# Optimization experiments

Hardware: AMD Instinct MI355X
Metric: run time of the kernel (lower is better)

The kernel has to match this reference:

```python
import jax, jax.numpy as jnp
import numpy as np

D_MODEL, N_LAYER, VOCAB = 1024, 4, 50280
D_INNER, D_STATE, D_CONV, DT_RANK = 2048, 16, 4, 64
B, L = 1, 1024
EPS = 1e-5


def _rmsnorm(x, w):
    var = jnp.mean(jnp.square(x), axis=-1, keepdims=True)
    return x * jax.lax.rsqrt(var + EPS) * w


def _selective_scan(u, dt, A, Bm, Cm, Dv):
    # u, dt: [b,l,d]; A: [d,n]; Bm, Cm: [b,l,n]; Dv: [d]
    dA = jnp.exp(dt[..., None] * A)                      # [b,l,d,n]
    dBu = dt[..., None] * Bm[:, :, None, :] * u[..., None]  # [b,l,d,n]

    def step(s, x):
        dA_t, dBu_t, C_t = x
        s = s * dA_t + dBu_t                             # [b,d,n]
        y = jnp.einsum('bdn,bn->bd', s, C_t)
        return s, y

    s0 = jnp.zeros((u.shape[0], u.shape[2], A.shape[1]), u.dtype)
    xs = (dA.transpose(1, 0, 2, 3), dBu.transpose(1, 0, 2, 3), Cm.transpose(1, 0, 2))
    _, ys = jax.lax.scan(step, s0, xs)                   # ys: [l,b,d]
    return ys.transpose(1, 0, 2) + u * Dv


def _mixer(x, in_w, cw, cb, xp_w, dt_w, dt_b, A_log, Dv, out_w):
    Lx = x.shape[1]
    xz = jnp.einsum('bld,ed->ble', x, in_w)              # [b,l,2*d_inner]
    xp, z = jnp.split(xz, 2, axis=-1)
    # causal depthwise conv1d, kernel size D_CONV
    xpad = jnp.pad(xp, ((0, 0), (D_CONV - 1, 0), (0, 0)))
    conv = cb + sum(xpad[:, k:k + Lx, :] * cw[:, k] for k in range(D_CONV))
    u = jax.nn.silu(conv)
    xdbl = jnp.einsum('bld,ed->ble', u, xp_w)            # [b,l,dt_rank+2n]
    dt_r = xdbl[..., :DT_RANK]
    Bm = xdbl[..., DT_RANK:DT_RANK + D_STATE]
    Cm = xdbl[..., DT_RANK + D_STATE:]
    dt = jax.nn.softplus(jnp.einsum('blr,dr->bld', dt_r, dt_w) + dt_b)
    A = -jnp.exp(A_log)
    y = _selective_scan(u, dt, A, Bm, Cm, Dv)
    y = y * jax.nn.silu(z)
    return jnp.einsum('bld,ed->ble', y, out_w)


def _forward(input_ids, embedding, norm_w, in_proj_w, conv_w, conv_b, x_proj_w,
             dt_proj_w, dt_proj_b, A_log, D, out_proj_w, norm_f_w):
    hidden = embedding[input_ids]                        # [b,l,d_model]
    residual = None
    for i in range(N_LAYER):
        residual = hidden if residual is None else hidden + residual
        x = _rmsnorm(residual, norm_w[i])
        hidden = _mixer(x, in_proj_w[i], conv_w[i], conv_b[i], x_proj_w[i],
                        dt_proj_w[i], dt_proj_b[i], A_log[i], D[i], out_proj_w[i])
    residual = hidden + residual
    hf = _rmsnorm(residual, norm_f_w)
    # lm_head weight is tied to embedding
    return jnp.einsum('bld,vd->blv', hf, embedding)


def setup_inputs() -> dict:
    key = jax.random.key(0)
    ks = jax.random.split(key, 8)
    s = 0.02
    return {
        'input_ids': jax.random.randint(ks[0], (B, L), 0, VOCAB),
        'embedding': jax.random.normal(ks[1], (VOCAB, D_MODEL), jnp.float32) * s,
        'norm_w': jnp.ones((N_LAYER, D_MODEL), jnp.float32),
        'in_proj_w': jax.random.normal(ks[2], (N_LAYER, 2 * D_INNER, D_MODEL), jnp.float32) * s,
        'conv_w': jax.random.normal(ks[3], (N_LAYER, D_INNER, D_CONV), jnp.float32) * s,
        'conv_b': jnp.zeros((N_LAYER, D_INNER), jnp.float32),
        'x_proj_w': jax.random.normal(ks[4], (N_LAYER, DT_RANK + 2 * D_STATE, D_INNER), jnp.float32) * s,
        'dt_proj_w': jax.random.normal(ks[5], (N_LAYER, D_INNER, DT_RANK), jnp.float32) * s,
        'dt_proj_b': jnp.full((N_LAYER, D_INNER), -4.6, jnp.float32),  # softplus ~= 0.01
        'A_log': jnp.tile(jnp.log(jnp.arange(1.0, D_STATE + 1.0, dtype=jnp.float32))[None, None, :],
                          (N_LAYER, D_INNER, 1)),
        'D': jnp.ones((N_LAYER, D_INNER), jnp.float32),
        'out_proj_w': jax.random.normal(ks[6], (N_LAYER, D_MODEL, D_INNER), jnp.float32) * s,
        'norm_f_w': jnp.ones((D_MODEL,), jnp.float32),
    }


def reference(input_ids, embedding, norm_w, in_proj_w, conv_w, conv_b, x_proj_w,
              dt_proj_w, dt_proj_b, A_log, D, out_proj_w, norm_f_w):
    return _forward(input_ids, embedding, norm_w, in_proj_w, conv_w, conv_b,
                    x_proj_w, dt_proj_w, dt_proj_b, A_log, D, out_proj_w, norm_f_w)
```

## Files before the change

### kernel.cpp

```cpp
#include <hip/hip_runtime.h>
#include <hip/hip_bf16.h>

#define D_MODEL 1024
#define N_LAYER 4
#define D_INNER 2048
#define D_STATE 16
#define D_CONV  4
#define DT_RANK 64
#define SEQ_L   1024
#define VOCAB   50280
#define VOCAB_PAD 50304
#define NCHUNK  32
#define CLEN    32

typedef __attribute__((ext_vector_type(8))) short short8;
typedef __attribute__((ext_vector_type(4))) float f32x4;

typedef __attribute__((address_space(1))) const unsigned GUint;
typedef __attribute__((address_space(3))) unsigned LUint;

__device__ __forceinline__ float silu_f(float x) {
    return x / (1.0f + __expf(-x));
}
__device__ __forceinline__ float softplus_f(float x) {
    return fmaxf(x, 0.0f) + log1pf(__expf(-fabsf(x)));
}
__device__ __forceinline__ ushort f2bf(float f) {
    union { float f; unsigned u; } uf; uf.f = f;
    unsigned r = uf.u + 0x7FFF + ((uf.u >> 16) & 1);
    return (ushort)(r >> 16);
}

__global__ void f32_to_bf16_kernel(const float* __restrict__ in,
                                   ushort* __restrict__ out, int n4) {
    int i = blockIdx.x * 256 + threadIdx.x;
    if (i >= n4) return;
    float4 v = *(const float4*)(in + (size_t)i * 4);
    ushort4 o;
    o.x = f2bf(v.x); o.y = f2bf(v.y); o.z = f2bf(v.z); o.w = f2bf(v.w);
    *(ushort4*)(out + (size_t)i * 4) = o;
}

__global__ void xpw_convert_kernel(const float* __restrict__ src,
                                   ushort* __restrict__ dst) {
    int q = blockIdx.x * 256 + threadIdx.x;
    int layer = q / (128 * 512);
    int rq    = q % (128 * 512);
    int row   = rq / 512;
    int cq    = rq % 512;
    ushort4 o;
    if (row < 96) {
        float4 v = *(const float4*)(src + ((size_t)layer * 96 + row) * 2048 + cq * 4);
        o.x = f2bf(v.x); o.y = f2bf(v.y); o.z = f2bf(v.z); o.w = f2bf(v.w);
    } else {
        o.x = o.y = o.z = o.w = 0;
    }
    *(ushort4*)(dst + (size_t)q * 4) = o;
}

__global__ void embed_kernel(const int* __restrict__ ids,
                             const float* __restrict__ emb,
                             float* __restrict__ hidden) {
    int l = blockIdx.x;
    int t = threadIdx.x;
    int id = ids[l];
    float4 v = *(const float4*)(emb + (size_t)id * D_MODEL + t * 4);
    *(float4*)(hidden + (size_t)l * D_MODEL + t * 4) = v;
}

__global__ void add_rmsnorm_kernel(float* __restrict__ res,
                                   const float* __restrict__ part,
                                   const float* __restrict__ w,
                                   ushort* __restrict__ xout,
                                   int add, int nparts) {
    int l = blockIdx.x;
    int t = threadIdx.x;
    size_t base = (size_t)l * D_MODEL + t * 4;
    float4 r;
    if (add) r = *(const float4*)(res + base);
    else     r = make_float4(0.f, 0.f, 0.f, 0.f);
    for (int s = 0; s < nparts; ++s) {
        float4 hv = *(const float4*)(part + (size_t)s * SEQ_L * D_MODEL + base);
        r.x += hv.x; r.y += hv.y; r.z += hv.z; r.w += hv.w;
    }
    *(float4*)(res + base) = r;
    float ss = r.x * r.x + r.y * r.y + r.z * r.z + r.w * r.w;
    #pragma unroll
    for (int off = 32; off > 0; off >>= 1) ss += __shfl_down(ss, off, 64);
    __shared__ float sred[4];
    if ((t & 63) == 0) sred[t >> 6] = ss;
    __syncthreads();
    float tot = sred[0] + sred[1] + sred[2] + sred[3];
    float scale = rsqrtf(tot * (1.0f / (float)D_MODEL) + 1e-5f);
    float4 wv = *(const float4*)(w + t * 4);
    ushort4 o;
    o.x = f2bf(r.x * scale * wv.x);
    o.y = f2bf(r.y * scale * wv.y);
    o.z = f2bf(r.z * scale * wv.z);
    o.w = f2bf(r.w * scale * wv.w);
    *(ushort4*)(xout + base) = o;
}

template<int SPLIT>
__global__ void gemm_bf16_gld_kernel(const ushort* __restrict__ A,
                                     const ushort* __restrict__ W,
                                     float* __restrict__ C,
                                     int N, int K, int lda, int ldc,
                                     int MB, int KS, int pstride) {
    __shared__ ushort As[2][128][32];
    __shared__ ushort Ws[2][128][32];
    const int t  = threadIdx.x;
    const int T  = gridDim.x >> 3;
    const int id = blockIdx.x;
    const int j  = (id & 7) * T + (id >> 3);
    const int ks  = j % KS;
    const int rem = j / KS;
    const int m0 = (rem % MB) * 128;
    const int n0 = (rem / MB) * 128;
    const int kchunk = K / KS;
    const int kbeg = ks * kchunk;
    const int kend = kbeg + kchunk;

    const int lane = t & 63;
    const int w    = t >> 6;
    const int srow = w * 16 + (lane >> 2);
    const int scol = (((lane & 3) ^ ((lane >> 3) & 3)) * 8);
    const ushort* Ag0 = A + (size_t)(m0 + srow) * lda + scol;
    const ushort* Ag1 = A + (size_t)(m0 + srow + 64) * lda + scol;
    const ushort* Wg0 = W + (size_t)(n0 + srow) * K + scol;
    const ushort* Wg1 = W + (size_t)(n0 + srow + 64) * K + scol;

    const int wm = (t >> 7) & 1;
    const int wn = (t >> 6) & 1;
    const int lr = lane & 15;
    const int lk = lane >> 4;
    const int swz = (lr >> 1) & 3;

    f32x4 acc[4][4] = {};

#define STAGE_GLD(buf, kk)                                                        \
    do {                                                                          \
        __builtin_amdgcn_global_load_lds((GUint*)(Ag0 + (kk)),                    \
            (LUint*)&As[buf][w * 16][0], 16, 0, 0);                               \
        __builtin_amdgcn_global_load_lds((GUint*)(Ag1 + (kk)),                    \
            (LUint*)&As[buf][64 + w * 16][0], 16, 0, 0);                          \
        __builtin_amdgcn_global_load_lds((GUint*)(Wg0 + (kk)),                    \
            (LUint*)&Ws[buf][w * 16][0], 16, 0, 0);                               \
        __builtin_amdgcn_global_load_lds((GUint*)(Wg1 + (kk)),                    \
            (LUint*)&Ws[buf][64 + w * 16][0], 16, 0, 0);                          \
    } while (0)

    STAGE_GLD(0, kbeg);
    int buf = 0;
    for (int k0 = kbeg;;) {
        __syncthreads();
        const bool more = (k0 + 32) < kend;
        if (more) STAGE_GLD(buf ^ 1, k0 + 32);

        short8 af[4], bfr[4];
        #pragma unroll
        for (int m = 0; m < 4; ++m)
            af[m] = *(const short8*)&As[buf][wm * 64 + m * 16 + lr][(lk ^ swz) * 8];
        #pragma unroll
        for (int n = 0; n < 4; ++n)
            bfr[n] = *(const short8*)&Ws[buf][wn * 64 + n * 16 + lr][(lk ^ swz) * 8];
        #pragma unroll
        for (int m = 0; m < 4; ++m)
            #pragma unroll
            for (int n = 0; n < 4; ++n)
                acc[m][n] = __builtin_amdgcn_mfma_f32_16x16x32_bf16(
                    af[m], bfr[n], acc[m][n], 0, 0, 0);

        if (!more) break;
        buf ^= 1;
        k0 += 32;
    }
#undef STAGE_GLD

    float* Cp = SPLIT ? (C + (size_t)ks * pstride) : C;
    #pragma unroll
    for (int m = 0; m < 4; ++m) {
        const int row = m0 + wm * 64 + m * 16 + lk * 4;
        #pragma unroll
        for (int n = 0; n < 4; ++n) {
            const int col = n0 + wn * 64 + n * 16 + lr;
            if (col < N) {
                #pragma unroll
                for (int r = 0; r < 4; ++r)
                    Cp[(size_t)(row + r) * ldc + col] = acc[m][n][r];
            }
        }
    }
}

__global__ void xdbl_reduce_kernel(const float* __restrict__ part,
                                   float* __restrict__ out,
                                   ushort* __restrict__ dtr_b) {
    int i = blockIdx.x * 256 + threadIdx.x;
    float4 acc = make_float4(0.f, 0.f, 0.f, 0.f);
    #pragma unroll
    for (int s = 0; s < 32; ++s) {
        float4 v = *(const float4*)(part + (size_t)s * SEQ_L * 96 + (size_t)i * 4);
        acc.x += v.x; acc.y += v.y; acc.z += v.z; acc.w += v.w;
    }
    *(float4*)(out + (size_t)i * 4) = acc;
    int c = (i * 4) % 96;
    if (c < 64) {
        int r = (i * 4) / 96;
        ushort4 o;
        o.x = f2bf(acc.x); o.y = f2bf(acc.y); o.z = f2bf(acc.z); o.w = f2bf(acc.w);
        *(ushort4*)(dtr_b + (size_t)r * 64 + c) = o;
    }
}

__global__ void conv_silu_kernel(const float* __restrict__ xz,
                                 const float* __restrict__ cw,
                                 const float* __restrict__ cb,
                                 float* __restrict__ u,
                                 ushort* __restrict__ u_b) {
    int idx = blockIdx.x * 256 + threadIdx.x;
    int l = idx >> 11;
    int c = idx & 2047;
    float acc = cb[c];
    float w0 = cw[c * 4 + 0], w1 = cw[c * 4 + 1], w2 = cw[c * 4 + 2], w3 = cw[c * 4 + 3];
#define XP(ll) (xz[(size_t)(ll) * 4096 + c] + xz[(size_t)SEQ_L * 4096 + (size_t)(ll) * 4096 + c])
    if (l >= 3) acc = fmaf(XP(l - 3), w0, acc);
    if (l >= 2) acc = fmaf(XP(l - 2), w1, acc);
    if (l >= 1) acc = fmaf(XP(l - 1), w2, acc);
    acc = fmaf(XP(l), w3, acc);
#undef XP
    float s = silu_f(acc);
    u[idx] = s;
    u_b[idx] = f2bf(s);
}

__global__ void scan_a_kernel(const float* __restrict__ u,
                              const float* __restrict__ dtp,
                              const float* __restrict__ dt_bias,
                              const float* __restrict__ xdbl,
                              const float* __restrict__ A_log,
                              float* __restrict__ yloc,
                              float* __restrict__ cumdt,
                              float* __restrict__ s_end) {
    const int idx = blockIdx.x * 256 + threadIdx.x;
    const int d = idx & 2047;
    const int c = idx >> 11;

    float Aa[16];
    #pragma unroll
    for (int q = 0; q < 4; ++q) {
        float4 al = *(const float4*)(A_log + (size_t)d * 16 + q * 4);
        Aa[q * 4 + 0] = -__expf(al.x);
        Aa[q * 4 + 1] = -__expf(al.y);
        Aa[q * 4 + 2] = -__expf(al.z);
        Aa[q * 4 + 3] = -__expf(al.w);
    }
    const float dbias = dt_bias[d];

    float s[16];
    #pragma unroll
    for (int n = 0; n < 16; ++n) s[n] = 0.0f;
    float cd = 0.0f;

    const int l0 = c * CLEN;
    for (int i = 0; i < CLEN; ++i) {
        const int l = l0 + i;
        const float dtl = softplus_f(dtp[(size_t)l * 2048 + d]
                                   + dtp[(size_t)SEQ_L * 2048 + (size_t)l * 2048 + d]
                                   + dbias);
        const float ul  = u[(size_t)l * 2048 + d];
        float Bn[16], Cn[16];
        const float* xbp = xdbl + (size_t)l * 96;
        *(float4*)&Bn[0]  = *(const float4*)(xbp + 64);
        *(float4*)&Bn[4]  = *(const float4*)(xbp + 68);
        *(float4*)&Bn[8]  = *(const float4*)(xbp + 72);
        *(float4*)&Bn[12] = *(const float4*)(xbp + 76);
        *(float4*)&Cn[0]  = *(const float4*)(xbp + 80);
        *(float4*)&Cn[4]  = *(const float4*)(xbp + 84);
        *(float4*)&Cn[8]  = *(const float4*)(xbp + 88);
        *(float4*)&Cn[12] = *(const float4*)(xbp + 92);
        cd += dtl;
        const float dtu = dtl * ul;
        float y = 0.0f;
        #pragma unroll
        for (int n = 0; n < 16; ++n) {
            float dA = __expf(dtl * Aa[n]);
            s[n] = fmaf(s[n], dA, dtu * Bn[n]);
            y = fmaf(s[n], Cn[n], y);
        }
        yloc[(size_t)l * 4096 + d] = y;
        cumdt[(size_t)l * 2048 + d] = cd;
    }
    float* se = s_end + ((size_t)d * NCHUNK + c) * 16;
    #pragma unroll
    for (int q = 0; q < 4; ++q)
        *(float4*)(se + q * 4) = make_float4(s[q * 4], s[q * 4 + 1], s[q * 4 + 2], s[q * 4 + 3]);
}

__global__ void scan_b_kernel(const float* __restrict__ s_end,
                              const float* __restrict__ cumdt,
                              const float* __restrict__ A_log,
                              float* __restrict__ s_in) {
    const int idx = blockIdx.x * 256 + threadIdx.x;
    const int d = idx >> 4;
    const int n = idx & 15;
    const float Aa = -__expf(A_log[(size_t)d * 16 + n]);
    float s = 0.0f;
    #pragma unroll
    for (int c = 0; c < NCHUNK; ++c) {
        s_in[((size_t)d * NCHUNK + c) * 16 + n] = s;
        const float tot = cumdt[(size_t)(c * CLEN + CLEN - 1) * 2048 + d];
        s = s_end[((size_t)d * NCHUNK + c) * 16 + n] + __expf(Aa * tot) * s;
    }
}

__global__ void scan_c_kernel(const float* __restrict__ u,
                              const float* __restrict__ xdbl,
                              const float* __restrict__ A_log,
                              const float* __restrict__ Dv,
                              const float* __restrict__ xz,
                              const float* __restrict__ cumdt,
                              const float* __restrict__ s_in,
                              ushort* __restrict__ yb) {
    const int idx = blockIdx.x * 256 + threadIdx.x;
    const int l = idx >> 11;
    const int d = idx & 2047;
    const int c = l >> 5;

    const float cd = cumdt[idx];
    const float ul = u[idx];
    const float yv = xz[(size_t)l * 4096 + d];
    const float zv = xz[(size_t)l * 4096 + 2048 + d]
                   + xz[(size_t)SEQ_L * 4096 + (size_t)l * 4096 + 2048 + d];
    const float* Cp = xdbl + (size_t)l * 96 + 80;
    const float* si = s_in + ((size_t)d * NCHUNK + c) * 16;

    float corr = 0.0f;
    #pragma unroll
    for (int q = 0; q < 4; ++q) {
        float4 al = *(const float4*)(A_log + (size_t)d * 16 + q * 4);
        float4 cv = *(const float4*)(Cp + q * 4);
        float4 sv = *(const float4*)(si + q * 4);
        corr = fmaf(cv.x * __expf(-__expf(al.x) * cd), sv.x, corr);
        corr = fmaf(cv.y * __expf(-__expf(al.y) * cd), sv.y, corr);
        corr = fmaf(cv.z * __expf(-__expf(al.z) * cd), sv.z, corr);
        corr = fmaf(cv.w * __expf(-__expf(al.w) * cd), sv.w, corr);
    }
    const float y = (yv + corr + Dv[d] * ul) * silu_f(zv);
    yb[idx] = f2bf(y);
}

extern "C" void kernel_launch(void* const* d_in, const int* in_sizes, int n_in,
                              void* d_out, int out_size, void* d_ws, size_t ws_size,
                              hipStream_t stream) {
    const int*   ids        = (const int*)d_in[0];
    const float* emb        = (const float*)d_in[1];
    const float* norm_w     = (const float*)d_in[2];
    const float* in_proj_w  = (const float*)d_in[3];
    const float* conv_w     = (const float*)d_in[4];
    const float* conv_b     = (const float*)d_in[5];
    const float* x_proj_w   = (const float*)d_in[6];
    const float* dt_proj_w  = (const float*)d_in[7];
    const float* dt_proj_b  = (const float*)d_in[8];
    const float* A_log      = (const float*)d_in[9];
    const float* Dv         = (const float*)d_in[10];
    const float* out_proj_w = (const float*)d_in[11];
    const float* norm_f_w   = (const float*)d_in[12];
    float* out = (float*)d_out;

    char* p = (char*)d_ws;
    ushort* emb_b  = (ushort*)p; p += (size_t)VOCAB_PAD * D_MODEL * 2;
    ushort* inw_b  = (ushort*)p; p += (size_t)N_LAYER * 4096 * 1024 * 2;
    ushort* outw_b = (ushort*)p; p += (size_t)N_LAYER * 1024 * 2048 * 2;
    ushort* xpw_b  = (ushort*)p; p += (size_t)N_LAYER * 128 * 2048 * 2;
    ushort* dtw_b  = (ushort*)p; p += (size_t)N_LAYER * 2048 * 64 * 2;
    float* residual = (float*)p; p += (size_t)SEQ_L * D_MODEL * 4;
    float* hpart    = (float*)p; p += (size_t)8 * SEQ_L * D_MODEL * 4;
    float* scratch  = (float*)p; p += (size_t)2 * SEQ_L * 2048 * 4;
    float* xdbl     = (float*)p; p += (size_t)SEQ_L * 96 * 4;
    ushort* dtr_b   = (ushort*)p; p += (size_t)SEQ_L * 64 * 2;
    ushort* xb      = (ushort*)p; p += (size_t)SEQ_L * D_MODEL * 2;
    float* xzp      = (float*)p; p += (size_t)2 * SEQ_L * 4096 * 4;
    float* u        = (float*)p; p += (size_t)SEQ_L * 2048 * 4;
    ushort* u_b     = (ushort*)p; p += (size_t)SEQ_L * 2048 * 2;
    ushort* yb      = (ushort*)p; p += (size_t)SEQ_L * 2048 * 2;
    float* cumdt    = (float*)p; p += (size_t)SEQ_L * 2048 * 4;
    float* s_end    = (float*)p; p += (size_t)D_INNER * NCHUNK * 16 * 4;
    float* s_in     = (float*)p; p += (size_t)D_INNER * NCHUNK * 16 * 4;

    dim3 blk(256);

    f32_to_bf16_kernel<<<dim3(VOCAB * D_MODEL / 4 / 256), blk, 0, stream>>>(
        emb, emb_b, VOCAB * D_MODEL / 4);
    f32_to_bf16_kernel<<<dim3(N_LAYER * 4096 * 1024 / 4 / 256), blk, 0, stream>>>(
        in_proj_w, inw_b, N_LAYER * 4096 * 1024 / 4);
    f32_to_bf16_kernel<<<dim3(N_LAYER * 1024 * 2048 / 4 / 256), blk, 0, stream>>>(
        out_proj_w, outw_b, N_LAYER * 1024 * 2048 / 4);
    f32_to_bf16_kernel<<<dim3(N_LAYER * 2048 * 64 / 4 / 256), blk, 0, stream>>>(
        dt_proj_w, dtw_b, N_LAYER * 2048 * 64 / 4);
    xpw_convert_kernel<<<dim3(N_LAYER * 128 * 2048 / 4 / 256), blk, 0, stream>>>(
        x_proj_w, xpw_b);

    embed_kernel<<<dim3(SEQ_L), blk, 0, stream>>>(ids, emb, hpart);

    for (int i = 0; i < N_LAYER; ++i) {
        add_rmsnorm_kernel<<<dim3(SEQ_L), blk, 0, stream>>>(
            residual, hpart, norm_w + (size_t)i * D_MODEL, xb,
            i == 0 ? 0 : 1, i == 0 ? 1 : 8);

        gemm_bf16_gld_kernel<1><<<dim3(512), blk, 0, stream>>>(
            xb, inw_b + (size_t)i * 4096 * 1024, xzp, 4096, 1024, 1024, 4096,
            8, 2, SEQ_L * 4096);

        conv_silu_kernel<<<dim3(SEQ_L * D_INNER / 256), blk, 0, stream>>>(
            xzp, conv_w + (size_t)i * D_INNER * D_CONV, conv_b + (size_t)i * D_INNER,
            u, u_b);

        gemm_bf16_gld_kernel<1><<<dim3(256), blk, 0, stream>>>(
            u_b, xpw_b + (size_t)i * 128 * 2048, scratch, 96, 2048, 2048, 96,
            8, 32, SEQ_L * 96);
        xdbl_reduce_kernel<<<dim3(SEQ_L * 96 / 4 / 256), blk, 0, stream>>>(
            scratch, xdbl, dtr_b);

        gemm_bf16_gld_kernel<1><<<dim3(256), blk, 0, stream>>>(
            dtr_b, dtw_b + (size_t)i * 2048 * 64, scratch, 2048, 64, 64, 2048,
            8, 2, SEQ_L * 2048);

        scan_a_kernel<<<dim3(D_INNER * NCHUNK / 256), blk, 0, stream>>>(
            u, scratch, dt_proj_b + (size_t)i * D_INNER, xdbl,
            A_log + (size_t)i * D_INNER * D_STATE, xzp, cumdt, s_end);
        scan_b_kernel<<<dim3(D_INNER * 16 / 256), blk, 0, stream>>>(
            s_end, cumdt, A_log + (size_t)i * D_INNER * D_STATE, s_in);
        scan_c_kernel<<<dim3(SEQ_L * D_INNER / 256), blk, 0, stream>>>(
            u, xdbl, A_log + (size_t)i * D_INNER * D_STATE,
            Dv + (size_t)i * D_INNER, xzp, cumdt, s_in, yb);

        gemm_bf16_gld_kernel<1><<<dim3(512), blk, 0, stream>>>(
            yb, outw_b + (size_t)i * 1024 * 2048, hpart, 1024, 2048, 2048, 1024,
            8, 8, SEQ_L * D_MODEL);
    }

    add_rmsnorm_kernel<<<dim3(SEQ_L), blk, 0, stream>>>(
        residual, hpart, norm_f_w, xb, 1, 8);

    gemm_bf16_gld_kernel<0><<<dim3(3144), blk, 0, stream>>>(
        xb, emb_b, out, VOCAB, 1024, 1024, VOCAB, 8, 1, 0);
}
```

Baseline: 839.1 us.

## Fuse dt softplus into GEMM epilogue, cut split-K, double scan chunks

Adds a bias+softplus epilogue to the GEMM so dt_proj writes the final dt directly, and scan_a no longer sums split partials or applies softplus. Split-K factors are reduced: in_proj runs without split (removing the partial sums in conv and scan_c), x_proj goes from 32 to 16 splits, out_proj from 8 to 4. The scan chunk count doubles (64 chunks of 16) to give scan_a more parallelism, at the cost of a longer sequential scan_b. Fewer grid blocks on the GEMMs may lower occupancy on the large-K cases.

```diff
diff --git a/kernel.cpp b/kernel.cpp
--- a/kernel.cpp
+++ b/kernel.cpp
@@ -10,8 +10,8 @@
 #define SEQ_L   1024
 #define VOCAB   50280
 #define VOCAB_PAD 50304
-#define NCHUNK  32
-#define CLEN    32
+#define NCHUNK  64
+#define CLEN    16
 
 typedef __attribute__((ext_vector_type(8))) short short8;
 typedef __attribute__((ext_vector_type(4))) float f32x4;
@@ -101,10 +101,11 @@
     *(ushort4*)(xout + base) = o;
 }
 
-template<int SPLIT>
+template<int SPLIT, int EPI>
 __global__ void gemm_bf16_gld_kernel(const ushort* __restrict__ A,
                                      const ushort* __restrict__ W,
                                      float* __restrict__ C,
+                                     const float* __restrict__ bias,
                                      int N, int K, int lda, int ldc,
                                      int MB, int KS, int pstride) {
     __shared__ ushort As[2][128][32];
@@ -185,9 +186,13 @@
         for (int n = 0; n < 4; ++n) {
             const int col = n0 + wn * 64 + n * 16 + lr;
             if (col < N) {
+                const float bv = EPI ? bias[col] : 0.0f;
                 #pragma unroll
-                for (int r = 0; r < 4; ++r)
-                    Cp[(size_t)(row + r) * ldc + col] = acc[m][n][r];
+                for (int r = 0; r < 4; ++r) {
+                    float v = acc[m][n][r];
+                    if (EPI) v = softplus_f(v + bv);
+                    Cp[(size_t)(row + r) * ldc + col] = v;
+                }
             }
         }
     }
@@ -199,7 +204,7 @@
     int i = blockIdx.x * 256 + threadIdx.x;
     float4 acc = make_float4(0.f, 0.f, 0.f, 0.f);
     #pragma unroll
-    for (int s = 0; s < 32; ++s) {
+    for (int s = 0; s < 16; ++s) {
         float4 v = *(const float4*)(part + (size_t)s * SEQ_L * 96 + (size_t)i * 4);
         acc.x += v.x; acc.y += v.y; acc.z += v.z; acc.w += v.w;
     }
@@ -223,20 +228,17 @@
     int c = idx & 2047;
     float acc = cb[c];
     float w0 = cw[c * 4 + 0], w1 = cw[c * 4 + 1], w2 = cw[c * 4 + 2], w3 = cw[c * 4 + 3];
-#define XP(ll) (xz[(size_t)(ll) * 4096 + c] + xz[(size_t)SEQ_L * 4096 + (size_t)(ll) * 4096 + c])
-    if (l >= 3) acc = fmaf(XP(l - 3), w0, acc);
-    if (l >= 2) acc = fmaf(XP(l - 2), w1, acc);
-    if (l >= 1) acc = fmaf(XP(l - 1), w2, acc);
-    acc = fmaf(XP(l), w3, acc);
-#undef XP
+    if (l >= 3) acc = fmaf(xz[(size_t)(l - 3) * 4096 + c], w0, acc);
+    if (l >= 2) acc = fmaf(xz[(size_t)(l - 2) * 4096 + c], w1, acc);
+    if (l >= 1) acc = fmaf(xz[(size_t)(l - 1) * 4096 + c], w2, acc);
+    acc = fmaf(xz[(size_t)l * 4096 + c], w3, acc);
     float s = silu_f(acc);
     u[idx] = s;
     u_b[idx] = f2bf(s);
 }
 
 __global__ void scan_a_kernel(const float* __restrict__ u,
-                              const float* __restrict__ dtp,
-                              const float* __restrict__ dt_bias,
+                              const float* __restrict__ dt,
                               const float* __restrict__ xdbl,
                               const float* __restrict__ A_log,
                               float* __restrict__ yloc,
@@ -255,7 +257,6 @@
         Aa[q * 4 + 2] = -__expf(al.z);
         Aa[q * 4 + 3] = -__expf(al.w);
     }
-    const float dbias = dt_bias[d];
 
     float s[16];
     #pragma unroll
@@ -265,9 +266,7 @@
     const int l0 = c * CLEN;
     for (int i = 0; i < CLEN; ++i) {
         const int l = l0 + i;
-        const float dtl = softplus_f(dtp[(size_t)l * 2048 + d]
-                                   + dtp[(size_t)SEQ_L * 2048 + (size_t)l * 2048 + d]
-                                   + dbias);
+        const float dtl = dt[(size_t)l * 2048 + d];
         const float ul  = u[(size_t)l * 2048 + d];
         float Bn[16], Cn[16];
         const float* xbp = xdbl + (size_t)l * 96;
@@ -306,7 +305,7 @@
     const int n = idx & 15;
     const float Aa = -__expf(A_log[(size_t)d * 16 + n]);
     float s = 0.0f;
-    #pragma unroll
+    #pragma unroll 8
     for (int c = 0; c < NCHUNK; ++c) {
         s_in[((size_t)d * NCHUNK + c) * 16 + n] = s;
         const float tot = cumdt[(size_t)(c * CLEN + CLEN - 1) * 2048 + d];
@@ -325,13 +324,12 @@
     const int idx = blockIdx.x * 256 + threadIdx.x;
     const int l = idx >> 11;
     const int d = idx & 2047;
-    const int c = l >> 5;
+    const int c = l >> 4;
 
     const float cd = cumdt[idx];
     const float ul = u[idx];
     const float yv = xz[(size_t)l * 4096 + d];
-    const float zv = xz[(size_t)l * 4096 + 2048 + d]
-                   + xz[(size_t)SEQ_L * 4096 + (size_t)l * 4096 + 2048 + d];
+    const float zv = xz[(size_t)l * 4096 + 2048 + d];
     const float* Cp = xdbl + (size_t)l * 96 + 80;
     const float* si = s_in + ((size_t)d * NCHUNK + c) * 16;
 
@@ -375,14 +373,15 @@
     ushort* xpw_b  = (ushort*)p; p += (size_t)N_LAYER * 128 * 2048 * 2;
     ushort* dtw_b  = (ushort*)p; p += (size_t)N_LAYER * 2048 * 64 * 2;
     float* residual = (float*)p; p += (size_t)SEQ_L * D_MODEL * 4;
-    float* hpart    = (float*)p; p += (size_t)8 * SEQ_L * D_MODEL * 4;
-    float* scratch  = (float*)p; p += (size_t)2 * SEQ_L * 2048 * 4;
+    float* hpart    = (float*)p; p += (size_t)4 * SEQ_L * D_MODEL * 4;
+    float* xdpart   = (float*)p; p += (size_t)16 * SEQ_L * 96 * 4;
     float* xdbl     = (float*)p; p += (size_t)SEQ_L * 96 * 4;
     ushort* dtr_b   = (ushort*)p; p += (size_t)SEQ_L * 64 * 2;
     ushort* xb      = (ushort*)p; p += (size_t)SEQ_L * D_MODEL * 2;
-    float* xzp      = (float*)p; p += (size_t)2 * SEQ_L * 4096 * 4;
+    float* xz       = (float*)p; p += (size_t)SEQ_L * 4096 * 4;
     float* u        = (float*)p; p += (size_t)SEQ_L * 2048 * 4;
     ushort* u_b     = (ushort*)p; p += (size_t)SEQ_L * 2048 * 2;
+    float* dtb      = (float*)p; p += (size_t)SEQ_L * 2048 * 4;
     ushort* yb      = (ushort*)p; p += (size_t)SEQ_L * 2048 * 2;
     float* cumdt    = (float*)p; p += (size_t)SEQ_L * 2048 * 4;
     float* s_end    = (float*)p; p += (size_t)D_INNER * NCHUNK * 16 * 4;
@@ -406,43 +405,43 @@
     for (int i = 0; i < N_LAYER; ++i) {
         add_rmsnorm_kernel<<<dim3(SEQ_L), blk, 0, stream>>>(
             residual, hpart, norm_w + (size_t)i * D_MODEL, xb,
-            i == 0 ? 0 : 1, i == 0 ? 1 : 8);
-
-        gemm_bf16_gld_kernel<1><<<dim3(512), blk, 0, stream>>>(
-            xb, inw_b + (size_t)i * 4096 * 1024, xzp, 4096, 1024, 1024, 4096,
-            8, 2, SEQ_L * 4096);
+            i == 0 ? 0 : 1, i == 0 ? 1 : 4);
+
+        gemm_bf16_gld_kernel<0, 0><<<dim3(256), blk, 0, stream>>>(
+            xb, inw_b + (size_t)i * 4096 * 1024, xz, nullptr,
+            4096, 1024, 1024, 4096, 8, 1, 0);
 
         conv_silu_kernel<<<dim3(SEQ_L * D_INNER / 256), blk, 0, stream>>>(
-            xzp, conv_w + (size_t)i * D_INNER * D_CONV, conv_b + (size_t)i * D_INNER,
+            xz, conv_w + (size_t)i * D_INNER * D_CONV, conv_b + (size_t)i * D_INNER,
             u, u_b);
 
-        gemm_bf16_gld_kernel<1><<<dim3(256), blk, 0, stream>>>(
-            u_b, xpw_b + (size_t)i * 128 * 2048, scratch, 96, 2048, 2048, 96,
-            8, 32, SEQ_L * 96);
+        gemm_bf16_gld_kernel<1, 0><<<dim3(128), blk, 0, stream>>>(
+            u_b, xpw_b + (size_t)i * 128 * 2048, xdpart, nullptr,
+            96, 2048, 2048, 96, 8, 16, SEQ_L * 96);
         xdbl_reduce_kernel<<<dim3(SEQ_L * 96 / 4 / 256), blk, 0, stream>>>(
-            scratch, xdbl, dtr_b);
-
-        gemm_bf16_gld_kernel<1><<<dim3(256), blk, 0, stream>>>(
-            dtr_b, dtw_b + (size_t)i * 2048 * 64, scratch, 2048, 64, 64, 2048,
-            8, 2, SEQ_L * 2048);
+            xdpart, xdbl, dtr_b);
+
+        gemm_bf16_gld_kernel<0, 1><<<dim3(128), blk, 0, stream>>>(
+            dtr_b, dtw_b + (size_t)i * 2048 * 64, dtb,
+            dt_proj_b + (size_t)i * D_INNER,
+            2048, 64, 64, 2048, 8, 1, 0);
 
         scan_a_kernel<<<dim3(D_INNER * NCHUNK / 256), blk, 0, stream>>>(
-            u, scratch, dt_proj_b + (size_t)i * D_INNER, xdbl,
-            A_log + (size_t)i * D_INNER * D_STATE, xzp, cumdt, s_end);
+            u, dtb, xdbl, A_log + (size_t)i * D_INNER * D_STATE, xz, cumdt, s_end);
         scan_b_kernel<<<dim3(D_INNER * 16 / 256), blk, 0, stream>>>(
             s_end, cumdt, A_log + (size_t)i * D_INNER * D_STATE, s_in);
         scan_c_kernel<<<dim3(SEQ_L * D_INNER / 256), blk, 0, stream>>>(
             u, xdbl, A_log + (size_t)i * D_INNER * D_STATE,
-            Dv + (size_t)i * D_INNER, xzp, cumdt, s_in, yb);
-
-        gemm_bf16_gld_kernel<1><<<dim3(512), blk, 0, stream>>>(
-            yb, outw_b + (size_t)i * 1024 * 2048, hpart, 1024, 2048, 2048, 1024,
-            8, 8, SEQ_L * D_MODEL);
+            Dv + (size_t)i * D_INNER, xz, cumdt, s_in, yb);
+
+        gemm_bf16_gld_kernel<1, 0><<<dim3(256), blk, 0, stream>>>(
+            yb, outw_b + (size_t)i * 1024 * 2048, hpart, nullptr,
+            1024, 2048, 2048, 1024, 8, 4, SEQ_L * D_MODEL);
     }
 
     add_rmsnorm_kernel<<<dim3(SEQ_L), blk, 0, stream>>>(
-        residual, hpart, norm_f_w, xb, 1, 8);
-
-    gemm_bf16_gld_kernel<0><<<dim3(3144), blk, 0, stream>>>(
-        xb, emb_b, out, VOCAB, 1024, 1024, VOCAB, 8, 1, 0);
-}
+        residual, hpart, norm_f_w, xb, 1, 4);
+
+    gemm_bf16_gld_kernel<0, 0><<<dim3(3144), blk, 0, stream>>>(
+        xb, emb_b, out, nullptr, VOCAB, 1024, 1024, VOCAB, 8, 1, 0);
+}
```

Result: faster. 822.2 us (-2.0%).
